# Kernel tuning notes

Hardware: AMD Instinct MI355X
Metric: run time of the kernel (lower is better)

Reference implementation:

```python
import jax, jax.numpy as jnp
import numpy as np

N, E = 50000, 800000          # n_nodes, n_edges
IN_C, OUT_C = 128, 64         # in_channels, out_channels


def setup_inputs() -> dict:
    key = jax.random.key(0)
    ks = jax.random.split(key, 12)
    def w(k, i, o):
        return jax.random.normal(k, (i, o), jnp.float32) / np.float32(np.sqrt(i))
    return {
        "x": jax.random.normal(ks[0], (N, IN_C), jnp.float32),
        "edge_index": jax.random.randint(ks[1], (2, E), 0, N),
        "eps": jax.random.normal(ks[2], (N, OUT_C), jnp.float32),
        # encoder GCNConv1: in -> 2*out
        "W_e1": w(ks[3], IN_C, 2 * OUT_C), "b_e1": jnp.zeros((2 * OUT_C,), jnp.float32),
        # encoder GCNConv2: 2*out -> out
        "W_e2": w(ks[4], 2 * OUT_C, OUT_C), "b_e2": jnp.zeros((OUT_C,), jnp.float32),
        # fc_mu / fc_logvar: out -> out
        "W_mu": w(ks[5], OUT_C, OUT_C), "b_mu": jnp.zeros((OUT_C,), jnp.float32),
        "W_lv": w(ks[6], OUT_C, OUT_C), "b_lv": jnp.zeros((OUT_C,), jnp.float32),
        # decoder GCNConv1: out -> in
        "W_d1": w(ks[7], OUT_C, IN_C), "b_d1": jnp.zeros((IN_C,), jnp.float32),
        # decoder GCNConv2: in -> in
        "W_d2": w(ks[8], IN_C, IN_C), "b_d2": jnp.zeros((IN_C,), jnp.float32),
    }


def _gcn_norm(edge_index, n):
    # PyG gcn_norm: add self-loops, symmetric D^-1/2 A D^-1/2 normalization
    loop = jnp.arange(n)
    src = jnp.concatenate([edge_index[0], loop])
    dst = jnp.concatenate([edge_index[1], loop])
    deg = jax.ops.segment_sum(jnp.ones_like(dst, jnp.float32), dst, num_segments=n)
    dinv = jnp.where(deg > 0, deg ** -0.5, 0.0)
    norm = dinv[src] * dinv[dst]  # [E + N]
    return src, dst, norm


def _gcn_conv(x, W, b, src, dst, norm, n):
    h = x @ W                       # linear transform first (small channel dim)
    msg = h[src] * norm[:, None]    # gather + edge scaling
    return jax.ops.segment_sum(msg, dst, num_segments=n) + b  # scatter-add + bias


def reference(x, edge_index, eps, W_e1, b_e1, W_e2, b_e2, W_mu, b_mu, W_lv, b_lv, W_d1, b_d1, W_d2, b_d2):
    n = x.shape[0]
    src, dst, norm = _gcn_norm(edge_index, n)
    # encoder
    h = jax.nn.relu(_gcn_conv(x, W_e1, b_e1, src, dst, norm, n))
    h = _gcn_conv(h, W_e2, b_e2, src, dst, norm, n)
    mu = h @ W_mu + b_mu
    logvar = h @ W_lv + b_lv
    # reparameterize (training mode)
    z = mu + eps * jnp.exp(0.5 * logvar)
    # decoder
    d = jax.nn.relu(_gcn_conv(z, W_d1, b_d1, src, dst, norm, n))
    d = _gcn_conv(d, W_d2, b_d2, src, dst, norm, n)
    return (d, mu, logvar)
```

## Files before the change

### kernel.cpp

```cpp
#include <hip/hip_runtime.h>
#include <math.h>

typedef unsigned short u16;
typedef unsigned int u32;
typedef __attribute__((ext_vector_type(8))) short s16x8;
typedef __attribute__((ext_vector_type(4))) float f32x4;

__device__ __forceinline__ float bf2f(u16 u) { return __uint_as_float(((u32)u) << 16); }
__device__ __forceinline__ u16 f2bf(float f) {
    u32 u = __float_as_uint(f);
    return (u16)((u + 0x7fffu + ((u >> 16) & 1u)) >> 16);
}

union U4 { u32 u[4]; s16x8 v; };

__device__ __forceinline__ s16x8 pack_hi(f32x4 x0, f32x4 x1) {
    U4 r;
    r.u[0] = (__float_as_uint(x0.y) & 0xFFFF0000u) | (__float_as_uint(x0.x) >> 16);
    r.u[1] = (__float_as_uint(x0.w) & 0xFFFF0000u) | (__float_as_uint(x0.z) >> 16);
    r.u[2] = (__float_as_uint(x1.y) & 0xFFFF0000u) | (__float_as_uint(x1.x) >> 16);
    r.u[3] = (__float_as_uint(x1.w) & 0xFFFF0000u) | (__float_as_uint(x1.z) >> 16);
    return r.v;
}
__device__ __forceinline__ s16x8 pack_lo(f32x4 x0, f32x4 x1) {
    float e0 = x0.x - __uint_as_float(__float_as_uint(x0.x) & 0xFFFF0000u);
    float e1 = x0.y - __uint_as_float(__float_as_uint(x0.y) & 0xFFFF0000u);
    float e2 = x0.z - __uint_as_float(__float_as_uint(x0.z) & 0xFFFF0000u);
    float e3 = x0.w - __uint_as_float(__float_as_uint(x0.w) & 0xFFFF0000u);
    float e4 = x1.x - __uint_as_float(__float_as_uint(x1.x) & 0xFFFF0000u);
    float e5 = x1.y - __uint_as_float(__float_as_uint(x1.y) & 0xFFFF0000u);
    float e6 = x1.z - __uint_as_float(__float_as_uint(x1.z) & 0xFFFF0000u);
    float e7 = x1.w - __uint_as_float(__float_as_uint(x1.w) & 0xFFFF0000u);
    U4 r;
    r.u[0] = (__float_as_uint(e1) & 0xFFFF0000u) | (__float_as_uint(e0) >> 16);
    r.u[1] = (__float_as_uint(e3) & 0xFFFF0000u) | (__float_as_uint(e2) >> 16);
    r.u[2] = (__float_as_uint(e5) & 0xFFFF0000u) | (__float_as_uint(e4) >> 16);
    r.u[3] = (__float_as_uint(e7) & 0xFFFF0000u) | (__float_as_uint(e6) >> 16);
    return r.v;
}

#define BSHIFT 9
#define BSIZE 512
#define BCAP 10240


struct PackArgs { const float* w[6]; };

__global__ __launch_bounds__(256) void k_pack6(PackArgs pa, u16* __restrict__ out) {
    const int Ks[6] = {128, 128, 64, 64, 64, 128};
    const int Ms[6] = {128, 64, 64, 64, 128, 128};
    const int Off[6] = {0, 16384, 24576, 28672, 32768, 40960};
    int s = blockIdx.y;
    int K = Ks[s], M = Ms[s];
    int id = blockIdx.x * 256 + threadIdx.x;
    if (id >= K * M) return;
    int ms = (M == 128) ? 7 : 6;
    int k = id >> ms, c = id & (M - 1);
    int chunk = k >> 5, j = k & 7, lq = (k >> 3) & 3;
    int ct = c >> 4, ln = (c & 15) + (lq << 4);
    out[Off[s] + (chunk * (M >> 4) + ct) * 512 + ln * 8 + j] = f2bf(pa.w[s][id]);
}


__global__ __launch_bounds__(256) void k_bin(const int* __restrict__ ei, int E, int NB,
                                             int* __restrict__ bin_cursor, u32* __restrict__ binned) {
    __shared__ int hist[128];
    __shared__ int base_l[128];
    const int t = threadIdx.x;
    const int e0 = blockIdx.x * 4096;
    int sreg[16], dreg[16];
#pragma unroll
    for (int j = 0; j < 16; ++j) {
        int e = e0 + j * 256 + t;
        if (e < E) {
            sreg[j] = ei[e];
            dreg[j] = ei[E + e];
        } else {
            dreg[j] = -1;
        }
    }
    if (t < NB) hist[t] = 0;
    __syncthreads();
#pragma unroll
    for (int j = 0; j < 16; ++j)
        if (dreg[j] >= 0) atomicAdd(&hist[dreg[j] >> BSHIFT], 1);
    __syncthreads();
    if (t < NB) {
        base_l[t] = atomicAdd(&bin_cursor[t], hist[t]);
        hist[t] = 0;
    }
    __syncthreads();
#pragma unroll
    for (int j = 0; j < 16; ++j)
        if (dreg[j] >= 0) {
            int b = dreg[j] >> BSHIFT;
            int pos = base_l[b] + atomicAdd(&hist[b], 1);
            if (pos < BCAP) binned[(size_t)b * BCAP + pos] = ((u32)(dreg[j] & (BSIZE - 1)) << 17) | (u32)sreg[j];
        }
}


__global__ __launch_bounds__(256) void k_cnt_alloc(const u32* __restrict__ binned,
                                                   const int* __restrict__ bin_cursor, int N,
                                                   int* __restrict__ cnt, float* __restrict__ dinv,
                                                   int* __restrict__ row_start, int* __restrict__ cursor) {
    __shared__ int cnt_l[BSIZE];
    __shared__ int wave_sum[5];
    __shared__ int base_s;
    const int t = threadIdx.x;
    const int b = blockIdx.x;
    const int lane = t & 63, w = t >> 6;
    cnt_l[t] = 0;
    cnt_l[t + 256] = 0;
    __syncthreads();
    const int n = min(bin_cursor[b], BCAP);
    for (int i = t; i < n; i += 256) atomicAdd(&cnt_l[binned[(size_t)b * BCAP + i] >> 17], 1);
    __syncthreads();
    int c0 = cnt_l[2 * t], c1 = cnt_l[2 * t + 1];
    int p0 = (c0 + 7) & ~7, p1 = (c1 + 7) & ~7;
    int s = p0 + p1;
    int incl = s;
#pragma unroll
    for (int o = 1; o < 64; o <<= 1) {
        int v = __shfl_up(incl, o, 64);
        if (lane >= o) incl += v;
    }
    if (lane == 63) wave_sum[w] = incl;
    __syncthreads();
    if (t == 0) {
        int acc = 0;
#pragma unroll
        for (int i = 0; i < 4; ++i) {
            int v = wave_sum[i];
            wave_sum[i] = acc;
            acc += v;
        }
        base_s = atomicAdd(cursor, acc);
    }
    __syncthreads();
    int excl = incl - s + wave_sum[w] + base_s;
    int v0 = b * BSIZE + 2 * t;
    if (v0 < N) {
        cnt[v0] = c0;
        dinv[v0] = rsqrtf((float)(c0 + 1));
        row_start[v0] = excl;
    }
    if (v0 + 1 < N) {
        cnt[v0 + 1] = c1;
        dinv[v0 + 1] = rsqrtf((float)(c1 + 1));
        row_start[v0 + 1] = excl + p0;
    }
}


__global__ __launch_bounds__(256) void k_scatter(const u32* __restrict__ binned,
                                                 const int* __restrict__ bin_cursor,
                                                 const int* __restrict__ row_start, const int* __restrict__ cnt,
                                                 const float* __restrict__ dinv, int N,
                                                 int2* __restrict__ edges) {
    __shared__ float dv_l[BSIZE];
    __shared__ int rs_l[BSIZE];
    __shared__ int fill_l[BSIZE];
    const int t = threadIdx.x;
    const int b = blockIdx.x;
#pragma unroll
    for (int hh = 0; hh < 2; ++hh) {
        int d = t + hh * 256;
        int v = b * BSIZE + d;
        bool ok = v < N;
        dv_l[d] = ok ? dinv[v] : 0.f;
        rs_l[d] = ok ? row_start[v] : 0;
        fill_l[d] = 0;
    }
    __syncthreads();
    const int n = min(bin_cursor[b], BCAP);
    for (int i = t; i < n; i += 256) {
        u32 e = binned[(size_t)b * BCAP + i];
        int dl = e >> 17;
        int src = e & 0x1FFFF;
        float wgt = dinv[src] * dv_l[dl];
        int pos = rs_l[dl] + atomicAdd(&fill_l[dl], 1);
        edges[pos] = make_int2(src, __float_as_int(wgt));
    }
    __syncthreads();
#pragma unroll
    for (int hh = 0; hh < 2; ++hh) {
        int d = t + hh * 256;
        int v = b * BSIZE + d;
        if (v >= N) continue;
        int c = fill_l[d];
        int pc = (c + 7) & ~7;
        for (int j = c; j < pc; ++j) edges[rs_l[d] + j] = make_int2(0, 0);
    }
}


template <int K, int M, int RT, int NSET, bool XBF16, bool OUT_BF16, bool BREL>
__global__ __launch_bounds__(256, 3) void k_gemm(const void* __restrict__ Xv, const u16* __restrict__ Bpk,
                                                 const float* __restrict__ b0, const float* __restrict__ b1,
                                                 const float* __restrict__ eps,
                                                 void* __restrict__ Y0, float* __restrict__ Y1,
                                                 u16* __restrict__ Z, int N) {
    constexpr int CH = K / 32;
    constexpr int TPM = M >> 4;
    constexpr int SETSTRIDE = CH * TPM * 512;
    const int lane = threadIdx.x & 63, w = threadIdx.x >> 6;
    const int l15 = lane & 15, q = lane >> 4;
    const int col0 = blockIdx.x * 64;
    const int row0 = blockIdx.y * (RT * 64);

    s16x8 Bfr[NSET * CH * 4];
#pragma unroll
    for (int s = 0; s < NSET; ++s)
#pragma unroll
        for (int ch = 0; ch < CH; ++ch)
#pragma unroll
            for (int ct = 0; ct < 4; ++ct)
                Bfr[(s * CH + ch) * 4 + ct] =
                    *(const s16x8*)&Bpk[(size_t)s * SETSTRIDE + ((ch * TPM) + (col0 >> 4) + ct) * 512 + lane * 8];

    f32x4 acc[NSET][RT][4];
#pragma unroll
    for (int s = 0; s < NSET; ++s)
#pragma unroll
        for (int rt = 0; rt < RT; ++rt)
#pragma unroll
            for (int ct = 0; ct < 4; ++ct) acc[s][rt][ct] = 0.f;

#pragma unroll
    for (int ch = 0; ch < CH; ++ch) {
#pragma unroll
        for (int rt = 0; rt < RT; ++rt) {
            int r = row0 + (w * RT + rt) * 16 + l15;
            r = r < N ? r : N - 1;
            s16x8 ah, al;
            if (XBF16) {
                ah = *(const s16x8*)((const u16*)Xv + (size_t)r * K + (ch << 5) + (q << 3));
            } else {
                const float* xp = (const float*)Xv + (size_t)r * K + (ch << 5) + (q << 3);
                f32x4 x0 = *(const f32x4*)xp;
                f32x4 x1 = *(const f32x4*)(xp + 4);
                ah = pack_hi(x0, x1);
                al = pack_lo(x0, x1);
            }
#pragma unroll
            for (int s = 0; s < NSET; ++s)
#pragma unroll
                for (int ct = 0; ct < 4; ++ct) {
                    int fb = (s * CH + ch) * 4 + ct;
                    acc[s][rt][ct] = __builtin_amdgcn_mfma_f32_16x16x32_bf16(ah, Bfr[fb], acc[s][rt][ct], 0, 0, 0);
                    if (!XBF16)
                        acc[s][rt][ct] = __builtin_amdgcn_mfma_f32_16x16x32_bf16(al, Bfr[fb], acc[s][rt][ct], 0, 0, 0);
                }
        }
    }

#pragma unroll
    for (int rt = 0; rt < RT; ++rt)
#pragma unroll
        for (int ct = 0; ct < 4; ++ct)
#pragma unroll
            for (int reg = 0; reg < 4; ++reg) {
                int row = row0 + (w * RT + rt) * 16 + q * 4 + reg;
                if (row >= N) continue;
                int col = col0 + ct * 16 + l15;
                if (NSET == 1) {
                    float v = acc[0][rt][ct][reg];
                    if (BREL) v = fmaxf(v + b0[col], 0.f);
                    if (OUT_BF16)
                        ((u16*)Y0)[(size_t)row * M + col] = f2bf(v);
                    else
                        ((float*)Y0)[(size_t)row * M + col] = v;
                } else {
                    float mu = acc[0][rt][ct][reg] + b0[col];
                    float lv = acc[1][rt][ct][reg] + b1[col];
                    size_t o = (size_t)row * 64 + col;
                    ((float*)Y0)[o] = mu;
                    Y1[o] = lv;
                    Z[o] = f2bf(mu + eps[o] * expf(0.5f * lv));
                }
            }
}


template <bool RELU, bool OUT_BF16>
__global__ __launch_bounds__(256) void k_agg128(const u16* __restrict__ hin, const int2* __restrict__ edges,
                                                const int* __restrict__ row_start, const int* __restrict__ cnt,
                                                const float* __restrict__ dinv, const float* __restrict__ bias,
                                                void* __restrict__ out, int N) {
    const int v = blockIdx.x * 4 + (threadIdx.x >> 6);
    const int lane = threadIdx.x & 63;
    if (v >= N) return;
    const int start = __builtin_amdgcn_readfirstlane(row_start[v]);
    const int c = __builtin_amdgcn_readfirstlane(cnt[v]);
    const int pc = (c + 7) & ~7;
    const u32* hp = (const u32*)hin;
    float a0 = 0.f, a1 = 0.f;
    if (pc) {
        int2 e[8];
#pragma unroll
        for (int j = 0; j < 8; ++j) e[j] = edges[start + j];
        for (int i = 0; i < pc; i += 8) {
            u32 h[8];
            float wv[8];
#pragma unroll
            for (int j = 0; j < 8; ++j) {
                h[j] = hp[(size_t)e[j].x * 64 + lane];
                wv[j] = __int_as_float(e[j].y);
            }
            if (i + 8 < pc) {
#pragma unroll
                for (int j = 0; j < 8; ++j) e[j] = edges[start + i + 8 + j];
            }
#pragma unroll
            for (int j = 0; j < 8; ++j) {
                a0 = fmaf(wv[j], bf2f((u16)h[j]), a0);
                a1 = fmaf(wv[j], bf2f((u16)(h[j] >> 16)), a1);
            }
        }
    }
    float dv = dinv[v], sw = dv * dv;
    u32 hs = hp[(size_t)v * 64 + lane];
    a0 = fmaf(sw, bf2f((u16)hs), a0);
    a1 = fmaf(sw, bf2f((u16)(hs >> 16)), a1);
    float2 bp = ((const float2*)bias)[lane];
    a0 += bp.x;
    a1 += bp.y;
    if (RELU) { a0 = fmaxf(a0, 0.f); a1 = fmaxf(a1, 0.f); }
    if (OUT_BF16)
        ((u32*)out)[(size_t)v * 64 + lane] = (u32)f2bf(a0) | ((u32)f2bf(a1) << 16);
    else
        ((float2*)out)[(size_t)v * 64 + lane] = make_float2(a0, a1);
}

template <bool HASB>
__global__ __launch_bounds__(256) void k_agg64(const u16* __restrict__ hin, const int2* __restrict__ edges,
                                               const int* __restrict__ row_start, const int* __restrict__ cnt,
                                               const float* __restrict__ dinv, const float* __restrict__ bias,
                                               float* __restrict__ out, int N) {
    const int v = blockIdx.x * 4 + (threadIdx.x >> 6);
    const int lane = threadIdx.x & 63;
    if (v >= N) return;
    const int start = __builtin_amdgcn_readfirstlane(row_start[v]);
    const int c = __builtin_amdgcn_readfirstlane(cnt[v]);
    const int pc = (c + 7) & ~7;
    float a0 = 0.f;
    if (pc) {
        int2 e[8];
#pragma unroll
        for (int j = 0; j < 8; ++j) e[j] = edges[start + j];
        for (int i = 0; i < pc; i += 8) {
            u16 h[8];
            float wv[8];
#pragma unroll
            for (int j = 0; j < 8; ++j) {
                h[j] = hin[(size_t)e[j].x * 64 + lane];
                wv[j] = __int_as_float(e[j].y);
            }
            if (i + 8 < pc) {
#pragma unroll
                for (int j = 0; j < 8; ++j) e[j] = edges[start + i + 8 + j];
            }
#pragma unroll
            for (int j = 0; j < 8; ++j) a0 = fmaf(wv[j], bf2f(h[j]), a0);
        }
    }
    float dv = dinv[v];
    a0 = fmaf(dv * dv, bf2f(hin[(size_t)v * 64 + lane]), a0);
    if (HASB) a0 += bias[lane];
    out[(size_t)v * 64 + lane] = a0;
}


extern "C" void kernel_launch(void* const* d_in, const int* in_sizes, int n_in,
                              void* d_out, int out_size, void* d_ws, size_t ws_size,
                              hipStream_t stream) {
    const float* x = (const float*)d_in[0];
    const int* ei = (const int*)d_in[1];
    const float* eps = (const float*)d_in[2];
    const float* We1 = (const float*)d_in[3];
    const float* be1 = (const float*)d_in[4];
    const float* We2 = (const float*)d_in[5];
    const float* be2 = (const float*)d_in[6];
    const float* Wmu = (const float*)d_in[7];
    const float* bmu = (const float*)d_in[8];
    const float* Wlv = (const float*)d_in[9];
    const float* blv = (const float*)d_in[10];
    const float* Wd1 = (const float*)d_in[11];
    const float* bd1 = (const float*)d_in[12];
    const float* Wd2 = (const float*)d_in[13];
    const float* bd2 = (const float*)d_in[14];

    const int N = in_sizes[0] / 128;
    const int E = in_sizes[1] / 2;
    const int ECAP = E + 8 * N;
    const int NB = (N + BSIZE - 1) >> BSHIFT;

    int* bin_cursor = (int*)d_ws;
    int* cursor = bin_cursor + 128;
    float* dinv = (float*)(bin_cursor + 256);
    int* row_start = (int*)(dinv + N);
    int* cnt = row_start + N;
    int2* edges = (int2*)(cnt + N);
    u16* R1 = (u16*)(edges + ECAP);
    u16* AZu = R1 + (size_t)N * 128;
    float* AZf = (float*)AZu;
    u32* binned = (u32*)AZu;
    u16* Wpk = AZu + (size_t)N * 128;

    float* out_d = (float*)d_out;
    float* out_mu = out_d + (size_t)N * 128;
    float* out_lv = out_mu + (size_t)N * 64;
    float* H2 = out_d;

    hipMemsetAsync(d_ws, 0, 256 * 4, stream);

    PackArgs pa;
    pa.w[0] = We1; pa.w[1] = We2; pa.w[2] = Wmu; pa.w[3] = Wlv; pa.w[4] = Wd1; pa.w[5] = Wd2;
    k_pack6<<<dim3(64, 6), dim3(256), 0, stream>>>(pa, Wpk);

    k_bin<<<dim3((E + 4095) / 4096), dim3(256), 0, stream>>>(ei, E, NB, bin_cursor, binned);
    k_cnt_alloc<<<dim3(NB), dim3(256), 0, stream>>>(binned, bin_cursor, N, cnt, dinv, row_start, cursor);
    k_scatter<<<dim3(NB), dim3(256), 0, stream>>>(binned, bin_cursor, row_start, cnt, dinv, N, edges);

    const int RB128 = (N + 127) / 128;
    const int RB64 = (N + 63) / 64;
    const int AB = (N + 3) / 4;

    k_gemm<128, 128, 2, 1, false, true, false><<<dim3(2, RB128), dim3(256), 0, stream>>>(x, Wpk, nullptr, nullptr, nullptr, R1, nullptr, nullptr, N);
    k_agg128<true, true><<<dim3(AB), dim3(256), 0, stream>>>(R1, edges, row_start, cnt, dinv, be1, AZu, N);
    k_gemm<128, 64, 1, 1, true, true, false><<<dim3(1, RB64), dim3(256), 0, stream>>>(AZu, Wpk + 16384, nullptr, nullptr, nullptr, R1, nullptr, nullptr, N);
    k_agg64<true><<<dim3(AB), dim3(256), 0, stream>>>(R1, edges, row_start, cnt, dinv, be2, H2, N);
    k_gemm<64, 64, 1, 2, false, false, false><<<dim3(1, RB64), dim3(256), 0, stream>>>(H2, Wpk + 24576, bmu, blv, eps, out_mu, out_lv, R1, N);
    k_agg64<false><<<dim3(AB), dim3(256), 0, stream>>>(R1, edges, row_start, cnt, dinv, nullptr, AZf, N);
    k_gemm<64, 128, 2, 1, false, true, true><<<dim3(2, RB128), dim3(256), 0, stream>>>(AZf, Wpk + 32768, bd1, nullptr, nullptr, AZu, nullptr, nullptr, N);
    k_gemm<128, 128, 2, 1, true, true, false><<<dim3(2, RB128), dim3(256), 0, stream>>>(AZu, Wpk + 40960, nullptr, nullptr, nullptr, R1, nullptr, nullptr, N);
    k_agg128<false, false><<<dim3(AB), dim3(256), 0, stream>>>(R1, edges, row_start, cnt, dinv, bd2, out_d, N);
}
```

Baseline: 338.8 us.

## Fuse graph preprocessing kernels with weight packing and first GEMM halves

Merges weight packing into the edge-binning launch and splits the first 128x128 GEMM into two column halves that run as extra blocks inside the count/alloc and scatter launches. Independent work now shares launches, which cuts kernel count and fills idle CUs during the small preprocessing grids. The decoder intermediate moves to a new buffer B2 because AZu aliases the binned edge array, which is still live while the first GEMM runs. The costs are a larger workspace and heavier register and LDS use in the fused kernels, which may lower occupancy for the preprocessing blocks.

Measured after the change: 327.7 us. 1.03x faster.

```diff
diff --git a/kernel.cpp b/kernel.cpp
--- a/kernel.cpp
+++ b/kernel.cpp
@@ -43,16 +43,16 @@
 #define BSIZE 512
 #define BCAP 10240
 
-
 struct PackArgs { const float* w[6]; };
 
-__global__ __launch_bounds__(256) void k_pack6(PackArgs pa, u16* __restrict__ out) {
+
+__device__ __forceinline__ void pack_body(const PackArgs& pa, u16* __restrict__ out, int g, int t) {
     const int Ks[6] = {128, 128, 64, 64, 64, 128};
     const int Ms[6] = {128, 64, 64, 64, 128, 128};
     const int Off[6] = {0, 16384, 24576, 28672, 32768, 40960};
-    int s = blockIdx.y;
+    int s = g >> 6;
+    int id = (g & 63) * 256 + t;
     int K = Ks[s], M = Ms[s];
-    int id = blockIdx.x * 256 + threadIdx.x;
     if (id >= K * M) return;
     int ms = (M == 128) ? 7 : 6;
     int k = id >> ms, c = id & (M - 1);
@@ -62,11 +62,17 @@
 }
 
 
-__global__ __launch_bounds__(256) void k_bin(const int* __restrict__ ei, int E, int NB,
-                                             int* __restrict__ bin_cursor, u32* __restrict__ binned) {
-    __shared__ int hist[128];
-    __shared__ int base_l[128];
+__global__ __launch_bounds__(256) void k_bin_pack(const int* __restrict__ ei, int E, int NB, int C,
+                                                  int* __restrict__ bin_cursor, u32* __restrict__ binned,
+                                                  PackArgs pa, u16* __restrict__ wpk) {
+    __shared__ int sh[256];
     const int t = threadIdx.x;
+    if ((int)blockIdx.x >= C) {
+        pack_body(pa, wpk, blockIdx.x - C, t);
+        return;
+    }
+    int* hist = sh;
+    int* base_l = sh + 128;
     const int e0 = blockIdx.x * 4096;
     int sreg[16], dreg[16];
 #pragma unroll
@@ -100,114 +106,17 @@
 }
 
 
-__global__ __launch_bounds__(256) void k_cnt_alloc(const u32* __restrict__ binned,
-                                                   const int* __restrict__ bin_cursor, int N,
-                                                   int* __restrict__ cnt, float* __restrict__ dinv,
-                                                   int* __restrict__ row_start, int* __restrict__ cursor) {
-    __shared__ int cnt_l[BSIZE];
-    __shared__ int wave_sum[5];
-    __shared__ int base_s;
-    const int t = threadIdx.x;
-    const int b = blockIdx.x;
-    const int lane = t & 63, w = t >> 6;
-    cnt_l[t] = 0;
-    cnt_l[t + 256] = 0;
-    __syncthreads();
-    const int n = min(bin_cursor[b], BCAP);
-    for (int i = t; i < n; i += 256) atomicAdd(&cnt_l[binned[(size_t)b * BCAP + i] >> 17], 1);
-    __syncthreads();
-    int c0 = cnt_l[2 * t], c1 = cnt_l[2 * t + 1];
-    int p0 = (c0 + 7) & ~7, p1 = (c1 + 7) & ~7;
-    int s = p0 + p1;
-    int incl = s;
-#pragma unroll
-    for (int o = 1; o < 64; o <<= 1) {
-        int v = __shfl_up(incl, o, 64);
-        if (lane >= o) incl += v;
-    }
-    if (lane == 63) wave_sum[w] = incl;
-    __syncthreads();
-    if (t == 0) {
-        int acc = 0;
-#pragma unroll
-        for (int i = 0; i < 4; ++i) {
-            int v = wave_sum[i];
-            wave_sum[i] = acc;
-            acc += v;
-        }
-        base_s = atomicAdd(cursor, acc);
-    }
-    __syncthreads();
-    int excl = incl - s + wave_sum[w] + base_s;
-    int v0 = b * BSIZE + 2 * t;
-    if (v0 < N) {
-        cnt[v0] = c0;
-        dinv[v0] = rsqrtf((float)(c0 + 1));
-        row_start[v0] = excl;
-    }
-    if (v0 + 1 < N) {
-        cnt[v0 + 1] = c1;
-        dinv[v0 + 1] = rsqrtf((float)(c1 + 1));
-        row_start[v0 + 1] = excl + p0;
-    }
-}
-
-
-__global__ __launch_bounds__(256) void k_scatter(const u32* __restrict__ binned,
-                                                 const int* __restrict__ bin_cursor,
-                                                 const int* __restrict__ row_start, const int* __restrict__ cnt,
-                                                 const float* __restrict__ dinv, int N,
-                                                 int2* __restrict__ edges) {
-    __shared__ float dv_l[BSIZE];
-    __shared__ int rs_l[BSIZE];
-    __shared__ int fill_l[BSIZE];
-    const int t = threadIdx.x;
-    const int b = blockIdx.x;
-#pragma unroll
-    for (int hh = 0; hh < 2; ++hh) {
-        int d = t + hh * 256;
-        int v = b * BSIZE + d;
-        bool ok = v < N;
-        dv_l[d] = ok ? dinv[v] : 0.f;
-        rs_l[d] = ok ? row_start[v] : 0;
-        fill_l[d] = 0;
-    }
-    __syncthreads();
-    const int n = min(bin_cursor[b], BCAP);
-    for (int i = t; i < n; i += 256) {
-        u32 e = binned[(size_t)b * BCAP + i];
-        int dl = e >> 17;
-        int src = e & 0x1FFFF;
-        float wgt = dinv[src] * dv_l[dl];
-        int pos = rs_l[dl] + atomicAdd(&fill_l[dl], 1);
-        edges[pos] = make_int2(src, __float_as_int(wgt));
-    }
-    __syncthreads();
-#pragma unroll
-    for (int hh = 0; hh < 2; ++hh) {
-        int d = t + hh * 256;
-        int v = b * BSIZE + d;
-        if (v >= N) continue;
-        int c = fill_l[d];
-        int pc = (c + 7) & ~7;
-        for (int j = c; j < pc; ++j) edges[rs_l[d] + j] = make_int2(0, 0);
-    }
-}
-
-
 template <int K, int M, int RT, int NSET, bool XBF16, bool OUT_BF16, bool BREL>
-__global__ __launch_bounds__(256, 3) void k_gemm(const void* __restrict__ Xv, const u16* __restrict__ Bpk,
-                                                 const float* __restrict__ b0, const float* __restrict__ b1,
-                                                 const float* __restrict__ eps,
-                                                 void* __restrict__ Y0, float* __restrict__ Y1,
-                                                 u16* __restrict__ Z, int N) {
+__device__ __forceinline__ void gemm_tile(const void* __restrict__ Xv, const u16* __restrict__ Bpk,
+                                          const float* __restrict__ b0, const float* __restrict__ b1,
+                                          const float* __restrict__ eps,
+                                          void* __restrict__ Y0, float* __restrict__ Y1,
+                                          u16* __restrict__ Z, int N, int col0, int row0, int t) {
     constexpr int CH = K / 32;
     constexpr int TPM = M >> 4;
     constexpr int SETSTRIDE = CH * TPM * 512;
-    const int lane = threadIdx.x & 63, w = threadIdx.x >> 6;
+    const int lane = t & 63, w = t >> 6;
     const int l15 = lane & 15, q = lane >> 4;
-    const int col0 = blockIdx.x * 64;
-    const int row0 = blockIdx.y * (RT * 64);
 
     s16x8 Bfr[NSET * CH * 4];
 #pragma unroll
@@ -282,6 +191,125 @@
             }
 }
 
+template <int K, int M, int RT, int NSET, bool XBF16, bool OUT_BF16, bool BREL>
+__global__ __launch_bounds__(256, 3) void k_gemm(const void* __restrict__ Xv, const u16* __restrict__ Bpk,
+                                                 const float* __restrict__ b0, const float* __restrict__ b1,
+                                                 const float* __restrict__ eps,
+                                                 void* __restrict__ Y0, float* __restrict__ Y1,
+                                                 u16* __restrict__ Z, int N) {
+    gemm_tile<K, M, RT, NSET, XBF16, OUT_BF16, BREL>(Xv, Bpk, b0, b1, eps, Y0, Y1, Z, N,
+                                                     blockIdx.x * 64, blockIdx.y * (RT * 64), threadIdx.x);
+}
+
+
+__global__ __launch_bounds__(256, 3) void k_cnt_gemm1(const u32* __restrict__ binned,
+                                                      const int* __restrict__ bin_cursor, int N, int NB,
+                                                      int* __restrict__ cnt, float* __restrict__ dinv,
+                                                      int* __restrict__ row_start, int* __restrict__ cursor,
+                                                      const float* __restrict__ x, const u16* __restrict__ wpk,
+                                                      u16* __restrict__ R1) {
+    __shared__ int cnt_l[BSIZE];
+    __shared__ int wave_sum[5];
+    __shared__ int base_s;
+    const int t = threadIdx.x;
+    const int b = blockIdx.x;
+    if (b >= NB) {
+        gemm_tile<128, 128, 2, 1, false, true, false>(x, wpk, nullptr, nullptr, nullptr, R1, nullptr, nullptr,
+                                                      N, 0, (b - NB) * 128, t);
+        return;
+    }
+    const int lane = t & 63, w = t >> 6;
+    cnt_l[t] = 0;
+    cnt_l[t + 256] = 0;
+    __syncthreads();
+    const int n = min(bin_cursor[b], BCAP);
+    for (int i = t; i < n; i += 256) atomicAdd(&cnt_l[binned[(size_t)b * BCAP + i] >> 17], 1);
+    __syncthreads();
+    int c0 = cnt_l[2 * t], c1 = cnt_l[2 * t + 1];
+    int p0 = (c0 + 7) & ~7, p1 = (c1 + 7) & ~7;
+    int s = p0 + p1;
+    int incl = s;
+#pragma unroll
+    for (int o = 1; o < 64; o <<= 1) {
+        int v = __shfl_up(incl, o, 64);
+        if (lane >= o) incl += v;
+    }
+    if (lane == 63) wave_sum[w] = incl;
+    __syncthreads();
+    if (t == 0) {
+        int acc = 0;
+#pragma unroll
+        for (int i = 0; i < 4; ++i) {
+            int v = wave_sum[i];
+            wave_sum[i] = acc;
+            acc += v;
+        }
+        base_s = atomicAdd(cursor, acc);
+    }
+    __syncthreads();
+    int excl = incl - s + wave_sum[w] + base_s;
+    int v0 = b * BSIZE + 2 * t;
+    if (v0 < N) {
+        cnt[v0] = c0;
+        dinv[v0] = rsqrtf((float)(c0 + 1));
+        row_start[v0] = excl;
+    }
+    if (v0 + 1 < N) {
+        cnt[v0 + 1] = c1;
+        dinv[v0 + 1] = rsqrtf((float)(c1 + 1));
+        row_start[v0 + 1] = excl + p0;
+    }
+}
+
+
+__global__ __launch_bounds__(256, 3) void k_scat_gemm1(const u32* __restrict__ binned,
+                                                       const int* __restrict__ bin_cursor,
+                                                       const int* __restrict__ row_start,
+                                                       const float* __restrict__ dinv, int N, int NB,
+                                                       int2* __restrict__ edges,
+                                                       const float* __restrict__ x, const u16* __restrict__ wpk,
+                                                       u16* __restrict__ R1) {
+    __shared__ float dv_l[BSIZE];
+    __shared__ int rs_l[BSIZE];
+    __shared__ int fill_l[BSIZE];
+    const int t = threadIdx.x;
+    const int b = blockIdx.x;
+    if (b >= NB) {
+        gemm_tile<128, 128, 2, 1, false, true, false>(x, wpk, nullptr, nullptr, nullptr, R1, nullptr, nullptr,
+                                                      N, 64, (b - NB) * 128, t);
+        return;
+    }
+#pragma unroll
+    for (int hh = 0; hh < 2; ++hh) {
+        int d = t + hh * 256;
+        int v = b * BSIZE + d;
+        bool ok = v < N;
+        dv_l[d] = ok ? dinv[v] : 0.f;
+        rs_l[d] = ok ? row_start[v] : 0;
+        fill_l[d] = 0;
+    }
+    __syncthreads();
+    const int n = min(bin_cursor[b], BCAP);
+    for (int i = t; i < n; i += 256) {
+        u32 e = binned[(size_t)b * BCAP + i];
+        int dl = e >> 17;
+        int src = e & 0x1FFFF;
+        float wgt = dinv[src] * dv_l[dl];
+        int pos = rs_l[dl] + atomicAdd(&fill_l[dl], 1);
+        edges[pos] = make_int2(src, __float_as_int(wgt));
+    }
+    __syncthreads();
+#pragma unroll
+    for (int hh = 0; hh < 2; ++hh) {
+        int d = t + hh * 256;
+        int v = b * BSIZE + d;
+        if (v >= N) continue;
+        int c = fill_l[d];
+        int pc = (c + 7) & ~7;
+        for (int j = c; j < pc; ++j) edges[rs_l[d] + j] = make_int2(0, 0);
+    }
+}
+
 
 template <bool RELU, bool OUT_BF16>
 __global__ __launch_bounds__(256) void k_agg128(const u16* __restrict__ hin, const int2* __restrict__ edges,
@@ -395,6 +423,7 @@
     const int E = in_sizes[1] / 2;
     const int ECAP = E + 8 * N;
     const int NB = (N + BSIZE - 1) >> BSHIFT;
+    const int C = (E + 4095) / 4096;
 
     int* bin_cursor = (int*)d_ws;
     int* cursor = bin_cursor + 128;
@@ -404,9 +433,10 @@
     int2* edges = (int2*)(cnt + N);
     u16* R1 = (u16*)(edges + ECAP);
     u16* AZu = R1 + (size_t)N * 128;
+    u16* B2 = AZu + (size_t)N * 128;
+    u16* Wpk = B2 + (size_t)N * 128;
     float* AZf = (float*)AZu;
     u32* binned = (u32*)AZu;
-    u16* Wpk = AZu + (size_t)N * 128;
 
     float* out_d = (float*)d_out;
     float* out_mu = out_d + (size_t)N * 128;
@@ -417,23 +447,22 @@
 
     PackArgs pa;
     pa.w[0] = We1; pa.w[1] = We2; pa.w[2] = Wmu; pa.w[3] = Wlv; pa.w[4] = Wd1; pa.w[5] = Wd2;
-    k_pack6<<<dim3(64, 6), dim3(256), 0, stream>>>(pa, Wpk);
-
-    k_bin<<<dim3((E + 4095) / 4096), dim3(256), 0, stream>>>(ei, E, NB, bin_cursor, binned);
-    k_cnt_alloc<<<dim3(NB), dim3(256), 0, stream>>>(binned, bin_cursor, N, cnt, dinv, row_start, cursor);
-    k_scatter<<<dim3(NB), dim3(256), 0, stream>>>(binned, bin_cursor, row_start, cnt, dinv, N, edges);
 
     const int RB128 = (N + 127) / 128;
     const int RB64 = (N + 63) / 64;
     const int AB = (N + 3) / 4;
 
-    k_gemm<128, 128, 2, 1, false, true, false><<<dim3(2, RB128), dim3(256), 0, stream>>>(x, Wpk, nullptr, nullptr, nullptr, R1, nullptr, nullptr, N);
+    k_bin_pack<<<dim3(C + 384), dim3(256), 0, stream>>>(ei, E, NB, C, bin_cursor, binned, pa, Wpk);
+    k_cnt_gemm1<<<dim3(NB + RB128), dim3(256), 0, stream>>>(binned, bin_cursor, N, NB, cnt, dinv, row_start,
+                                                            cursor, x, Wpk, R1);
+    k_scat_gemm1<<<dim3(NB + RB128), dim3(256), 0, stream>>>(binned, bin_cursor, row_start, dinv, N, NB,
+                                                             edges, x, Wpk, R1);
     k_agg128<true, true><<<dim3(AB), dim3(256), 0, stream>>>(R1, edges, row_start, cnt, dinv, be1, AZu, N);
     k_gemm<128, 64, 1, 1, true, true, false><<<dim3(1, RB64), dim3(256), 0, stream>>>(AZu, Wpk + 16384, nullptr, nullptr, nullptr, R1, nullptr, nullptr, N);
     k_agg64<true><<<dim3(AB), dim3(256), 0, stream>>>(R1, edges, row_start, cnt, dinv, be2, H2, N);
     k_gemm<64, 64, 1, 2, false, false, false><<<dim3(1, RB64), dim3(256), 0, stream>>>(H2, Wpk + 24576, bmu, blv, eps, out_mu, out_lv, R1, N);
     k_agg64<false><<<dim3(AB), dim3(256), 0, stream>>>(R1, edges, row_start, cnt, dinv, nullptr, AZf, N);
-    k_gemm<64, 128, 2, 1, false, true, true><<<dim3(2, RB128), dim3(256), 0, stream>>>(AZf, Wpk + 32768, bd1, nullptr, nullptr, AZu, nullptr, nullptr, N);
-    k_gemm<128, 128, 2, 1, true, true, false><<<dim3(2, RB128), dim3(256), 0, stream>>>(AZu, Wpk + 40960, nullptr, nullptr, nullptr, R1, nullptr, nullptr, N);
+    k_gemm<64, 128, 2, 1, false, true, true><<<dim3(2, RB128), dim3(256), 0, stream>>>(AZf, Wpk + 32768, bd1, nullptr, nullptr, B2, nullptr, nullptr, N);
+    k_gemm<128, 128, 2, 1, true, true, false><<<dim3(2, RB128), dim3(256), 0, stream>>>(B2, Wpk + 40960, nullptr, nullptr, nullptr, R1, nullptr, nullptr, N);
     k_agg128<false, false><<<dim3(AB), dim3(256), 0, stream>>>(R1, edges, row_start, cnt, dinv, bd2, out_d, N);
 }
```
